# Optimization experiments

Hardware: AMD Instinct MI355X
Metric: run time of the kernel (lower is better)

The kernel has to match this reference:

```python
import jax, jax.numpy as jnp
from jax import lax
import numpy as np

NB_HEAD = 8
D_MODEL = 64
KERNEL = 3


def setup_inputs() -> dict:
    key = jax.random.key(0)
    k1, k2, k3, k4, k5 = jax.random.split(key, 5)
    B, N, T, D = 16, 1024, 24, D_MODEL
    value = jax.random.normal(k1, (B, N, T, D), dtype=jnp.float32)
    # Conv2d(d_model, d_model, (1, kernel_size)) weights (OIHW) + bias
    fan_in = D * 1 * KERNEL
    bound = 1.0 / np.sqrt(fan_in)
    W_conv = jax.random.uniform(k2, (D, D, 1, KERNEL), jnp.float32, -bound, bound)
    b_conv = jax.random.uniform(k3, (D,), jnp.float32, -bound, bound)
    # Linear(d_model, d_model): W (out, in), bias (out,)
    lb = 1.0 / np.sqrt(D)
    W_lin = jax.random.uniform(k4, (D, D), jnp.float32, -lb, lb)
    b_lin = jax.random.uniform(k5, (D,), jnp.float32, -lb, lb)
    return {"value": value, "W_conv": W_conv, "b_conv": b_conv,
            "W_lin": W_lin, "b_lin": b_lin}


def reference(value, W_conv, b_conv, W_lin, b_lin):
    B, N, T, D = value.shape
    h = NB_HEAD
    d_k = D // h
    pad = (KERNEL - 1) // 2
    # conv1D_aware_temporal_context1 on value.permute(0,3,1,2): (B, D, N, T)
    x = jnp.transpose(value, (0, 3, 1, 2))
    x = lax.conv_general_dilated(
        x, W_conv, window_strides=(1, 1), padding=[(0, 0), (pad, pad)],
        dimension_numbers=("NCHW", "OIHW", "NCHW"))
    x = x + b_conv[None, :, None, None]
    # view(B, h, d_k, N, T).permute(0,3,1,4,2) -> (B, N, h, T, d_k)
    v = jnp.transpose(x.reshape(B, h, d_k, N, T), (0, 3, 1, 4, 2))
    # relation_matrix_h is the tridiagonal all-ones band -> out[t] = v[t-1]+v[t]+v[t+1]
    vp = jnp.pad(v, ((0, 0), (0, 0), (0, 0), (1, 1), (0, 0)))
    v = vp[..., :-2, :] + vp[..., 1:-1, :] + vp[..., 2:, :]
    # transpose(2,3) then merge heads: (B, N, T, h*d_k)
    v = jnp.transpose(v, (0, 1, 3, 2, 4)).reshape(B, N, T, h * d_k)
    # linear_output1 + relu
    out = jax.nn.relu(jnp.einsum("bntd,od->bnto", v, W_lin) + b_lin)
    return out
```

## Files before the change

kernel.cpp:

```cpp
#include <hip/hip_runtime.h>
#include <hip/hip_bf16.h>


typedef __attribute__((ext_vector_type(8))) short short8;
typedef __attribute__((ext_vector_type(8))) __bf16 bf16x8;
typedef __attribute__((ext_vector_type(4))) float f4;

#define R_ROWS 8
#define VP_STRIDE 72
#define V_ROW_ELEMS (26 * VP_STRIDE)
#define W_STRIDE 200
#define Z_STRIDE 68

__device__ __forceinline__ unsigned short f2bfu(float f) {
    return __bfloat16_as_ushort(__float2bfloat16(f));
}

__global__ void prep_kernel(const float* __restrict__ Wconv,
                            const float* __restrict__ bconv,
                            const float* __restrict__ Wlin,
                            const float* __restrict__ blin,
                            __hip_bfloat16* __restrict__ wbig,
                            float* __restrict__ biasC,
                            float* __restrict__ blinF) {
    int idx = blockIdx.x * 256 + threadIdx.x;
    if (idx < 64 * 192) {
        int o = idx / 192;
        int j = idx - o * 192;
        int k = j >> 6;
        int i = j & 63;
        float acc = 0.0f;
        for (int c = 0; c < 64; ++c)
            acc += Wlin[o * 64 + c] * Wconv[c * 192 + i * 3 + k];
        wbig[o * 192 + j] = __float2bfloat16(acc);
    } else if (idx < 64 * 192 + 64) {
        int o = idx - 64 * 192;
        float acc = 0.0f;
        for (int c = 0; c < 64; ++c)
            acc += Wlin[o * 64 + c] * bconv[c];
        biasC[o] = acc;
    } else if (idx < 64 * 192 + 128) {
        int o = idx - (64 * 192 + 64);
        blinF[o] = blin[o];
    }
}

__global__ void fused_kernel(const float* __restrict__ value,
                             const __hip_bfloat16* __restrict__ wbig,
                             const float* __restrict__ biasC,
                             const float* __restrict__ blinF,
                             float* __restrict__ out) {
    __shared__ __align__(16) unsigned char smem[55552];
    short* Vlds = (short*)smem;
    short* Wlds = (short*)(smem + 29952);
    float* zbuf = (float*)smem;

    const int tid = threadIdx.x;
    const int wave = tid >> 6;
    const int lane = tid & 63;
    const int lane15 = lane & 15;
    const int quad = lane >> 4;
    const long base_row = (long)blockIdx.x * R_ROWS;

    for (int c4 = tid; c4 < 3072; c4 += 256) {
        int r = c4 / 384;
        int rem = c4 - r * 384;
        int t = rem >> 4;
        int d4 = (rem & 15) << 2;
        f4 v = *(const f4*)(value + (base_row + r) * 1536 + t * 64 + d4);
        ushort4 u;
        u.x = f2bfu(v.x); u.y = f2bfu(v.y); u.z = f2bfu(v.z); u.w = f2bfu(v.w);
        *(ushort4*)(Vlds + r * V_ROW_ELEMS + (t + 1) * VP_STRIDE + d4) = u;
    }
    if (tid < 128) {
        int r = tid >> 4;
        int which = (tid >> 3) & 1;
        int d8 = (tid & 7) << 3;
        uint4 z; z.x = 0; z.y = 0; z.z = 0; z.w = 0;
        *(uint4*)(Vlds + r * V_ROW_ELEMS + which * (25 * VP_STRIDE) + d8) = z;
    }
    const short* wsrc = (const short*)wbig;
    for (int c = tid; c < 1536; c += 256) {
        int n = c / 24;
        int k8 = (c - n * 24) << 3;
        *(uint4*)(Wlds + n * W_STRIDE + k8) = *(const uint4*)(wsrc + n * 192 + k8);
    }
    __syncthreads();

    f4 acc[3][4];
    #pragma unroll
    for (int a = 0; a < 3; ++a)
        #pragma unroll
        for (int b = 0; b < 4; ++b) {
            f4 zz = {0.f, 0.f, 0.f, 0.f};
            acc[a][b] = zz;
        }

    const int mt0 = wave * 3;
    int aoff[3];
    #pragma unroll
    for (int mt = 0; mt < 3; ++mt) {
        int m = (mt0 + mt) * 16 + lane15;
        int r = m / 24;
        int s = m - r * 24;
        aoff[mt] = r * V_ROW_ELEMS + s * VP_STRIDE;
    }
    const int k0 = quad * 8;
    #pragma unroll
    for (int ks = 0; ks < 6; ++ks) {
        int k = ks * 32 + k0;
        int ka = ((k >> 6) * VP_STRIDE) + (k & 63);
        bf16x8 bfr[4], afr[3];
        #pragma unroll
        for (int nt = 0; nt < 4; ++nt)
            bfr[nt] = __builtin_bit_cast(bf16x8,
                *(const short8*)(Wlds + nt * (16 * W_STRIDE) + lane15 * W_STRIDE + k));
        #pragma unroll
        for (int mt = 0; mt < 3; ++mt)
            afr[mt] = __builtin_bit_cast(bf16x8,
                *(const short8*)(Vlds + aoff[mt] + ka));
        #pragma unroll
        for (int mt = 0; mt < 3; ++mt)
            #pragma unroll
            for (int nt = 0; nt < 4; ++nt)
                acc[mt][nt] = __builtin_amdgcn_mfma_f32_16x16x32_bf16(
                    afr[mt], bfr[nt], acc[mt][nt], 0, 0, 0);
    }

    __syncthreads();
    #pragma unroll
    for (int mt = 0; mt < 3; ++mt) {
        int mbase = (mt0 + mt) * 16 + quad * 4;
        #pragma unroll
        for (int nt = 0; nt < 4; ++nt) {
            int o = nt * 16 + lane15;
            #pragma unroll
            for (int i = 0; i < 4; ++i)
                zbuf[(mbase + i) * Z_STRIDE + o] = acc[mt][nt][i];
        }
    }
    __syncthreads();

    for (int it = 0; it < 12; ++it) {
        int idx = it * 256 + tid;
        int o4 = (idx & 15) << 2;
        int tt = (idx >> 4) % 24;
        int r = idx / 384;
        int zrow = r * 24 + tt;
        f4 s = *(const f4*)(zbuf + zrow * Z_STRIDE + o4);
        float m = 3.0f;
        if (tt > 0)  { f4 p = *(const f4*)(zbuf + (zrow - 1) * Z_STRIDE + o4); s += p; }
        else m -= 1.0f;
        if (tt < 23) { f4 q = *(const f4*)(zbuf + (zrow + 1) * Z_STRIDE + o4); s += q; }
        else m -= 1.0f;
        f4 bc = *(const f4*)(biasC + o4);
        f4 bl = *(const f4*)(blinF + o4);
        f4 v = s + m * bc + bl;
        v.x = fmaxf(v.x, 0.0f);
        v.y = fmaxf(v.y, 0.0f);
        v.z = fmaxf(v.z, 0.0f);
        v.w = fmaxf(v.w, 0.0f);
        long orow = (base_row + r) * 24 + tt;
        *(f4*)(out + orow * 64 + o4) = v;
    }
}

extern "C" void kernel_launch(void* const* d_in, const int* in_sizes, int n_in,
                              void* d_out, int out_size, void* d_ws, size_t ws_size,
                              hipStream_t stream) {
    const float* value = (const float*)d_in[0];
    const float* Wconv = (const float*)d_in[1];
    const float* bconv = (const float*)d_in[2];
    const float* Wlin  = (const float*)d_in[3];
    const float* blin  = (const float*)d_in[4];
    float* out = (float*)d_out;

    __hip_bfloat16* wbig = (__hip_bfloat16*)d_ws;
    float* biasC = (float*)((char*)d_ws + 24576);
    float* blinF = (float*)((char*)d_ws + 24832);

    prep_kernel<<<49, 256, 0, stream>>>(Wconv, bconv, Wlin, blin, wbig, biasC, blinF);
    fused_kernel<<<2048, 256, 0, stream>>>(value, wbig, biasC, blinF, out);
}
```

Measured before the change: 210.8 us.

## Drop LDS weight staging and z-buffer; do temporal stencil in registers via shuffles

The fused kernel no longer stages the combined weight matrix in LDS. B fragments are read directly from global memory, where they should stay cache-resident. The z-buffer round trip through LDS is replaced by cross-lane shuffles that apply the 3-tap temporal sum in registers, and results are written straight to global memory. This shrinks LDS use to about 30KB and adds launch bounds for 4 blocks per CU to raise occupancy, at the cost of narrower scalar output stores instead of float4 stores. The prep kernel also caches W_lin in shared memory.

```diff
diff --git a/kernel.cpp b/kernel.cpp
--- a/kernel.cpp
+++ b/kernel.cpp
@@ -9,8 +9,6 @@
 #define R_ROWS 8
 #define VP_STRIDE 72
 #define V_ROW_ELEMS (26 * VP_STRIDE)
-#define W_STRIDE 200
-#define Z_STRIDE 68
 
 __device__ __forceinline__ unsigned short f2bfu(float f) {
     return __bfloat16_as_ushort(__float2bfloat16(f));
@@ -23,7 +21,11 @@
                             __hip_bfloat16* __restrict__ wbig,
                             float* __restrict__ biasC,
                             float* __restrict__ blinF) {
-    int idx = blockIdx.x * 256 + threadIdx.x;
+    __shared__ float Wl[4096];
+    const int tid = threadIdx.x;
+    for (int c = tid; c < 4096; c += 256) Wl[c] = Wlin[c];
+    __syncthreads();
+    int idx = blockIdx.x * 256 + tid;
     if (idx < 64 * 192) {
         int o = idx / 192;
         int j = idx - o * 192;
@@ -31,13 +33,13 @@
         int i = j & 63;
         float acc = 0.0f;
         for (int c = 0; c < 64; ++c)
-            acc += Wlin[o * 64 + c] * Wconv[c * 192 + i * 3 + k];
+            acc += Wl[o * 64 + c] * Wconv[c * 192 + i * 3 + k];
         wbig[o * 192 + j] = __float2bfloat16(acc);
     } else if (idx < 64 * 192 + 64) {
         int o = idx - 64 * 192;
         float acc = 0.0f;
         for (int c = 0; c < 64; ++c)
-            acc += Wlin[o * 64 + c] * bconv[c];
+            acc += Wl[o * 64 + c] * bconv[c];
         biasC[o] = acc;
     } else if (idx < 64 * 192 + 128) {
         int o = idx - (64 * 192 + 64);
@@ -45,15 +47,13 @@
     }
 }
 
-__global__ void fused_kernel(const float* __restrict__ value,
-                             const __hip_bfloat16* __restrict__ wbig,
-                             const float* __restrict__ biasC,
-                             const float* __restrict__ blinF,
-                             float* __restrict__ out) {
-    __shared__ __align__(16) unsigned char smem[55552];
-    short* Vlds = (short*)smem;
-    short* Wlds = (short*)(smem + 29952);
-    float* zbuf = (float*)smem;
+__global__ __launch_bounds__(256, 4) void fused_kernel(
+    const float* __restrict__ value,
+    const __hip_bfloat16* __restrict__ wbig,
+    const float* __restrict__ biasC,
+    const float* __restrict__ blinF,
+    float* __restrict__ out) {
+    __shared__ __align__(16) short Vlds[R_ROWS * V_ROW_ELEMS];
 
     const int tid = threadIdx.x;
     const int wave = tid >> 6;
@@ -79,12 +79,6 @@
         uint4 z; z.x = 0; z.y = 0; z.z = 0; z.w = 0;
         *(uint4*)(Vlds + r * V_ROW_ELEMS + which * (25 * VP_STRIDE) + d8) = z;
     }
-    const short* wsrc = (const short*)wbig;
-    for (int c = tid; c < 1536; c += 256) {
-        int n = c / 24;
-        int k8 = (c - n * 24) << 3;
-        *(uint4*)(Wlds + n * W_STRIDE + k8) = *(const uint4*)(wsrc + n * 192 + k8);
-    }
     __syncthreads();
 
     f4 acc[3][4];
@@ -105,6 +99,7 @@
         int s = m - r * 24;
         aoff[mt] = r * V_ROW_ELEMS + s * VP_STRIDE;
     }
+    const short* wsrc = (const short*)wbig;
     const int k0 = quad * 8;
     #pragma unroll
     for (int ks = 0; ks < 6; ++ks) {
@@ -114,7 +109,7 @@
         #pragma unroll
         for (int nt = 0; nt < 4; ++nt)
             bfr[nt] = __builtin_bit_cast(bf16x8,
-                *(const short8*)(Wlds + nt * (16 * W_STRIDE) + lane15 * W_STRIDE + k));
+                *(const short8*)(wsrc + (nt * 16 + lane15) * 192 + k));
         #pragma unroll
         for (int mt = 0; mt < 3; ++mt)
             afr[mt] = __builtin_bit_cast(bf16x8,
@@ -127,41 +122,46 @@
                     afr[mt], bfr[nt], acc[mt][nt], 0, 0, 0);
     }
 
-    __syncthreads();
+    float b3[4], b2[4];
+    #pragma unroll
+    for (int nt = 0; nt < 4; ++nt) {
+        int o = nt * 16 + lane15;
+        float bc = biasC[o];
+        float bl = blinF[o];
+        b3[nt] = 3.0f * bc + bl;
+        b2[nt] = 2.0f * bc + bl;
+    }
+    const int srcP = (lane + 48) & 63;
+    const int srcN = (lane + 16) & 63;
     #pragma unroll
     for (int mt = 0; mt < 3; ++mt) {
-        int mbase = (mt0 + mt) * 16 + quad * 4;
+        const int mtp = (mt > 0) ? mt - 1 : 0;
+        const int mtn = (mt < 2) ? mt + 1 : 2;
         #pragma unroll
         for (int nt = 0; nt < 4; ++nt) {
-            int o = nt * 16 + lane15;
+            float pin = __shfl(acc[mt][nt][3], srcP, 64);
+            float pxr = __shfl(acc[mtp][nt][3], srcP, 64);
+            float nin = __shfl(acc[mt][nt][0], srcN, 64);
+            float nxr = __shfl(acc[mtn][nt][0], srcN, 64);
+            float prev0 = (quad == 0) ? pxr : pin;
+            float next3 = (quad == 3) ? nxr : nin;
             #pragma unroll
-            for (int i = 0; i < 4; ++i)
-                zbuf[(mbase + i) * Z_STRIDE + o] = acc[mt][nt][i];
+            for (int i = 0; i < 4; ++i) {
+                int tq = mt * 16 + quad * 4 + i;
+                int rr = (tq >= 24) ? 1 : 0;
+                int t = tq - rr * 24;
+                float s = acc[mt][nt][i];
+                float prev = (i > 0) ? acc[mt][nt][i - 1] : prev0;
+                float next = (i < 3) ? acc[mt][nt][i + 1] : next3;
+                if (t > 0)  s += prev;
+                if (t < 23) s += next;
+                float bias = (t == 0 || t == 23) ? b2[nt] : b3[nt];
+                float r = fmaxf(s + bias, 0.0f);
+                long addr = ((base_row + 2 * wave + rr) * 24 + t) * 64
+                            + nt * 16 + lane15;
+                out[addr] = r;
+            }
         }
-    }
-    __syncthreads();
-
-    for (int it = 0; it < 12; ++it) {
-        int idx = it * 256 + tid;
-        int o4 = (idx & 15) << 2;
-        int tt = (idx >> 4) % 24;
-        int r = idx / 384;
-        int zrow = r * 24 + tt;
-        f4 s = *(const f4*)(zbuf + zrow * Z_STRIDE + o4);
-        float m = 3.0f;
-        if (tt > 0)  { f4 p = *(const f4*)(zbuf + (zrow - 1) * Z_STRIDE + o4); s += p; }
-        else m -= 1.0f;
-        if (tt < 23) { f4 q = *(const f4*)(zbuf + (zrow + 1) * Z_STRIDE + o4); s += q; }
-        else m -= 1.0f;
-        f4 bc = *(const f4*)(biasC + o4);
-        f4 bl = *(const f4*)(blinF + o4);
-        f4 v = s + m * bc + bl;
-        v.x = fmaxf(v.x, 0.0f);
-        v.y = fmaxf(v.y, 0.0f);
-        v.z = fmaxf(v.z, 0.0f);
-        v.w = fmaxf(v.w, 0.0f);
-        long orow = (base_row + r) * 24 + tt;
-        *(f4*)(out + orow * 64 + o4) = v;
     }
 }
 
```

New measurement: 209.1 us. About the same (-0.8%).
